# Kernel tuning notes

Hardware: AMD Instinct MI355X
Metric: run time of the kernel (lower is better)

Reference implementation:

```python
import jax, jax.numpy as jnp
import numpy as np

NEG_SLOPE = 0.2
EPS = 1e-16


def sp_gat_layer(h, src, trg, w, a_src, a_trg):
    # h: [N, f_in], w: [H, f_in, f_out], a_src/a_trg: [H, f_out]
    n = h.shape[0]
    h_prime = jnp.einsum('nf,hfo->nho', h, w)            # [N, H, O]
    attn_src = jnp.einsum('nho,ho->nh', h_prime, a_src)  # [N, H]
    attn_trg = jnp.einsum('nho,ho->nh', h_prime, a_trg)  # [N, H]
    e = jax.nn.leaky_relu(attn_src[src] + attn_trg[trg], NEG_SLOPE)  # [E, H]
    e = e - e.max()  # global max-shift, as in the torch code
    exp_e = jnp.exp(e)
    denom = jax.ops.segment_sum(exp_e, trg, num_segments=n)          # [N, H]
    neigh_attn = exp_e / (denom[trg] + EPS)                          # [E, H]
    h_weighted = h_prime[src] * neigh_attn[..., None]                # [E, H, O]
    return jax.ops.segment_sum(h_weighted, trg, num_segments=n)     # [N, H, O]


def run_stack(h, src, trg, params):
    # params: list of (w, a_src, a_trg); last layer mean over heads, others elu+flatten
    n = h.shape[0]
    n_layers = len(params)
    for i, (w, a_src, a_trg) in enumerate(params):
        out = sp_gat_layer(h, src, trg, w, a_src, a_trg)  # [N, H, O]
        if i + 1 == n_layers:
            h = out.mean(axis=1)                          # [N, O]
        else:
            h = jax.nn.elu(out.reshape(n, -1))            # [N, H*O]
    return h


def setup_inputs() -> dict:
    key = jax.random.key(0)
    ks = jax.random.split(key, 24)
    N, E = 60000, 800000
    H, F0, O = 8, 128, 32
    inp = {
        'h0': jax.random.normal(ks[0], (N, F0), jnp.float32),
        'h1': jax.random.normal(ks[1], (N, F0), jnp.float32),
        'src0': jax.random.randint(ks[2], (E,), 0, N),
        'trg0': jax.random.randint(ks[3], (E,), 0, N),
        'src1': jax.random.randint(ks[4], (E,), 0, N),
        'trg1': jax.random.randint(ks[5], (E,), 0, N),
        'w00': jax.random.normal(ks[6], (H, F0, O), jnp.float32) * 0.1,
        'asrc00': jax.random.normal(ks[7], (H, O), jnp.float32) * 0.1,
        'atrg00': jax.random.normal(ks[8], (H, O), jnp.float32) * 0.1,
        'w01': jax.random.normal(ks[9], (H, H * O, O), jnp.float32) * 0.1,
        'asrc01': jax.random.normal(ks[10], (H, O), jnp.float32) * 0.1,
        'atrg01': jax.random.normal(ks[11], (H, O), jnp.float32) * 0.1,
        'w10': jax.random.normal(ks[12], (H, F0, O), jnp.float32) * 0.1,
        'asrc10': jax.random.normal(ks[13], (H, O), jnp.float32) * 0.1,
        'atrg10': jax.random.normal(ks[14], (H, O), jnp.float32) * 0.1,
        'w11': jax.random.normal(ks[15], (H, H * O, O), jnp.float32) * 0.1,
        'asrc11': jax.random.normal(ks[16], (H, O), jnp.float32) * 0.1,
        'atrg11': jax.random.normal(ks[17], (H, O), jnp.float32) * 0.1,
        'fc_w': jax.random.normal(ks[18], (2 * O, 2), jnp.float32) * 0.1,
        'fc_b': jnp.zeros((2,), jnp.float32),
    }
    return inp


N_USER = 50000


def reference(h0, h1, src0, trg0, src1, trg1,
              w00, asrc00, atrg00, w01, asrc01, atrg01,
              w10, asrc10, atrg10, w11, asrc11, atrg11,
              fc_w, fc_b):
    emb0 = run_stack(h0, src0, trg0, [(w00, asrc00, atrg00), (w01, asrc01, atrg01)])
    emb1 = run_stack(h1, src1, trg1, [(w10, asrc10, atrg10), (w11, asrc11, atrg11)])
    ret = jnp.concatenate([emb0[:N_USER], emb1[:N_USER]], axis=-1)  # [n_user, 64]
    logits = ret @ fc_w + fc_b
    return jax.nn.log_softmax(logits, axis=-1)
```

## Files before the change

### kernel.cpp

```cpp
#include <hip/hip_runtime.h>
#include <math.h>

#define H 8
#define O 32
#define C 256
#define CAP 48
#define NEG_SLOPE 0.2f
#define EPS_V 1e-16f
#define LOG2E 1.4426950408889634f

#define W_BKT 128
#define NB_PAD 512
#define BCAP 2048
#define EPB 4096

typedef float f32x4 __attribute__((ext_vector_type(4)));
typedef float f32x2 __attribute__((ext_vector_type(2)));
typedef short bf16x8 __attribute__((ext_vector_type(8)));

__device__ __forceinline__ unsigned short f2bf(float x){
  unsigned u = __float_as_uint(x);
  unsigned r = (u + 0x7fffu + ((u >> 16) & 1u)) >> 16;
  return (unsigned short)r;
}

template<int F>
__device__ __forceinline__ void cvt_a_body(const float* __restrict__ src,
                                           short* __restrict__ dst,
                                           int n_nodes, int t, int total){
  constexpr int KB = F / 8;
  if (t >= total) return;
  int row = t / KB;
  int kb = t - row * KB;
  float v[8];
  if (row < n_nodes){
    const float4 p0 = *(const float4*)(src + (size_t)row * F + kb * 8);
    const float4 p1 = *(const float4*)(src + (size_t)row * F + kb * 8 + 4);
    v[0]=p0.x; v[1]=p0.y; v[2]=p0.z; v[3]=p0.w;
    v[4]=p1.x; v[5]=p1.y; v[6]=p1.z; v[7]=p1.w;
  } else {
    for (int j = 0; j < 8; ++j) v[j] = 0.f;
  }
  bf16x8 o;
  for (int j = 0; j < 8; ++j) o[j] = (short)f2bf(v[j]);
  *(bf16x8*)(dst + (size_t)t * 8) = o;
}

template<int F>
__device__ __forceinline__ void cvt_w_body(const float* __restrict__ w,
                                           short* __restrict__ wb, int t){
  constexpr int KB = F / 8;
  if (t >= 256 * KB) return;
  int c = t & 255, kb = t >> 8;
  int h = c >> 5, o = c & 31;
  bf16x8 out;
  for (int j = 0; j < 8; ++j){
    int f = kb * 8 + j;
    out[j] = (short)f2bf(w[((size_t)h * F + f) * O + o]);
  }
  *(bf16x8*)(wb + ((size_t)kb * 256 + c) * 8) = out;
}

__device__ void pass1_body(const int* __restrict__ trg, const int* __restrict__ src,
                           unsigned* __restrict__ gbuf, unsigned* __restrict__ gcur,
                           int E, int bx, int tid){
  __shared__ int cnt[NB_PAD];
  __shared__ int offl[NB_PAD];
  __shared__ unsigned baseg[NB_PAD];
  __shared__ int cur[NB_PAD];
  __shared__ unsigned payload[EPB];

  const int e0 = bx * EPB;
  const int ne = min(EPB, E - e0);
  for (int i = tid; i < NB_PAD; i += 256) cnt[i] = 0;
  __syncthreads();
  for (int i = tid; i < ne; i += 256){
    int t = trg[e0 + i];
    atomicAdd(&cnt[t >> 7], 1);
  }
  __syncthreads();
  for (int i = tid; i < NB_PAD; i += 256){
    int c = cnt[i];
    baseg[i] = c ? atomicAdd(&gcur[i], (unsigned)c) : 0u;
  }
  if (tid < 64){
    int v[8]; int s = 0;
#pragma unroll
    for (int j = 0; j < 8; ++j){ v[j] = cnt[tid * 8 + j]; s += v[j]; }
    int x = s;
#pragma unroll
    for (int d = 1; d < 64; d <<= 1){
      int o = __shfl_up(x, d, 64);
      if (tid >= d) x += o;
    }
    int base = x - s;
#pragma unroll
    for (int j = 0; j < 8; ++j){ offl[tid * 8 + j] = base; base += v[j]; }
  }
  __syncthreads();
  for (int i = tid; i < NB_PAD; i += 256) cur[i] = offl[i];
  __syncthreads();
  for (int i = tid; i < ne; i += 256){
    int t = trg[e0 + i];
    int s = src[e0 + i];
    int b = t >> 7;
    int p = atomicAdd(&cur[b], 1);
    payload[p] = ((unsigned)b << 23) | ((unsigned)(t & 127) << 16) | (unsigned)s;
  }
  __syncthreads();
  for (int i = tid; i < ne; i += 256){
    unsigned v = payload[i];
    unsigned b = v >> 23;
    unsigned pos = baseg[b] + (unsigned)(i - offl[b]);
    if (pos < BCAP) gbuf[(size_t)b * BCAP + pos] = v;
  }
}

__device__ void pass2_body(const unsigned* __restrict__ gbuf,
                           const unsigned* __restrict__ gcur,
                           unsigned short* __restrict__ csrc, int* __restrict__ degv,
                           int N, int bx, int tid){
  __shared__ unsigned short ell[W_BKT * CAP];
  __shared__ int dcnt[W_BKT];
  const int node0 = bx << 7;
  const int nn = min(W_BKT, N - node0);
  const unsigned pat = ((unsigned)N << 16) | (unsigned)N;
  unsigned* e32 = (unsigned*)ell;
  for (int i = tid; i < W_BKT * CAP / 2; i += 256) e32[i] = pat;
  for (int i = tid; i < W_BKT; i += 256) dcnt[i] = 0;
  __syncthreads();
  const int ne = min((int)gcur[bx], BCAP);
  for (int i = tid; i < ne; i += 256){
    unsigned v = gbuf[(size_t)bx * BCAP + i];
    int lt = (v >> 16) & 127;
    int p = atomicAdd(&dcnt[lt], 1);
    if (p < CAP) ell[lt * CAP + p] = (unsigned short)(v & 0xffffu);
  }
  __syncthreads();
  const uint4* s4 = (const uint4*)ell;
  uint4* d4 = (uint4*)(csrc + (size_t)node0 * CAP);
  const int n16 = nn * (CAP / 8);
  for (int i = tid; i < n16; i += 256) d4[i] = s4[i];
  for (int i = tid; i < nn; i += 256) degv[node0 + i] = dcnt[i];
}

template<int F>
__device__ __forceinline__ void gemm_body(
    const short* __restrict__ hb, const short* __restrict__ wb,
    const float* __restrict__ a_src, const float* __restrict__ a_trg,
    unsigned char* __restrict__ hp, float* __restrict__ as_, float* __restrict__ at_,
    int n_nodes, int bx, int tidx){
  constexpr int KB = F / 8;
  const int w = tidx >> 6, l = tidx & 63;
  const int q = l >> 4, m15 = l & 15;
  const int row0 = bx * 32;
  const int ct0 = w * 4;
  float wsv[4], wtv[4];
#pragma unroll
  for (int ct = 0; ct < 4; ++ct){
    int col = (ct0 + ct) * 16 + m15;
    wsv[ct] = a_src[col];
    wtv[ct] = a_trg[col];
  }
  f32x4 acc[2][4] = {};
#pragma unroll
  for (int kk = 0; kk < F / 32; ++kk){
    const int kb0 = kk * 4 + q;
    bf16x8 a0 = *(const bf16x8*)(hb + ((size_t)(row0 + m15) * KB + kb0) * 8);
    bf16x8 a1 = *(const bf16x8*)(hb + ((size_t)(row0 + 16 + m15) * KB + kb0) * 8);
    const short* wp = wb + ((size_t)kb0 * 256 + ct0 * 16 + m15) * 8;
#pragma unroll
    for (int ct = 0; ct < 4; ++ct){
      bf16x8 b = *(const bf16x8*)(wp + ct * 128);
      acc[0][ct] = __builtin_amdgcn_mfma_f32_16x16x32_bf16(a0, b, acc[0][ct], 0, 0, 0);
      acc[1][ct] = __builtin_amdgcn_mfma_f32_16x16x32_bf16(a1, b, acc[1][ct], 0, 0, 0);
    }
  }
#pragma unroll
  for (int rt2 = 0; rt2 < 2; ++rt2){
    int nb = row0 + rt2 * 16 + q * 4;
    float att[4][4] = {};
#pragma unroll
    for (int ct = 0; ct < 4; ++ct){
      int col = (ct0 + ct) * 16 + m15;
      int hi = ct >> 1;
      int p01 = __builtin_amdgcn_cvt_pk_fp8_f32(acc[rt2][ct][0], acc[rt2][ct][1], 0, false);
      int p23 = __builtin_amdgcn_cvt_pk_fp8_f32(acc[rt2][ct][2], acc[rt2][ct][3], 0, false);
      unsigned char qb[4] = {(unsigned char)(p01 & 0xff),
                             (unsigned char)((p01 >> 8) & 0xff),
                             (unsigned char)(p23 & 0xff),
                             (unsigned char)((p23 >> 8) & 0xff)};
#pragma unroll
      for (int r = 0; r < 4; ++r){
        int n = nb + r;
        if (n < n_nodes) hp[(size_t)n * C + col] = qb[r];
        float vr = acc[rt2][ct][r];
        att[r][hi]     = fmaf(vr, wsv[ct], att[r][hi]);
        att[r][2 + hi] = fmaf(vr, wtv[ct], att[r][2 + hi]);
      }
    }
#pragma unroll
    for (int r = 0; r < 4; ++r)
#pragma unroll
      for (int k = 0; k < 4; ++k){
        float v = att[r][k];
        v += __shfl_xor(v, 1, 64);
        v += __shfl_xor(v, 2, 64);
        v += __shfl_xor(v, 4, 64);
        v += __shfl_xor(v, 8, 64);
        att[r][k] = v;
      }
    if (m15 == 0){
      int h0i = 2 * w;
#pragma unroll
      for (int r = 0; r < 4; ++r){
        int n = nb + r;
        if (n < n_nodes){
          as_[n * H + h0i]     = att[r][0] * LOG2E;
          as_[n * H + h0i + 1] = att[r][1] * LOG2E;
          at_[n * H + h0i]     = att[r][2] * LOG2E;
          at_[n * H + h0i + 1] = att[r][3] * LOG2E;
        }
      }
    }
  }
}

__device__ __forceinline__ float gather_accum(
    const unsigned char* __restrict__ hp,
    const float* __restrict__ as_, float ath,
    const unsigned short* __restrict__ row, int deg, int l, int head,
    f32x2 (&acc)[4]){
  int degR = (deg + 7) & ~7;
  float dsum = 0.f;
  for (int jb = 0; jb < degR; jb += 8){
    ushort4 s4a = *(const ushort4*)(row + jb);
    ushort4 s4b = *(const ushort4*)(row + jb + 4);
    int ss[8] = {s4a.x, s4a.y, s4a.z, s4a.w, s4b.x, s4b.y, s4b.z, s4b.w};
    float xa[8];
#pragma unroll
    for (int i = 0; i < 8; ++i) xa[i] = as_[ss[i] * H + head];
    uint2 vv[8];
#pragma unroll
    for (int i = 0; i < 8; ++i)
      vv[i] = *(const uint2*)(hp + (size_t)ss[i] * C + l * 8);
#pragma unroll
    for (int i = 0; i < 8; ++i){
      float x = xa[i] + ath;
      x = fmaxf(x, NEG_SLOPE * x);
      float e = __builtin_amdgcn_exp2f(x);
      dsum += e;
      f32x2 ee = {e, e};
      f32x2 u0 = __builtin_amdgcn_cvt_pk_f32_fp8(vv[i].x, false);
      f32x2 u1 = __builtin_amdgcn_cvt_pk_f32_fp8(vv[i].x, true);
      f32x2 u2 = __builtin_amdgcn_cvt_pk_f32_fp8(vv[i].y, false);
      f32x2 u3 = __builtin_amdgcn_cvt_pk_f32_fp8(vv[i].y, true);
      acc[0] += u0 * ee;
      acc[1] += u1 * ee;
      acc[2] += u2 * ee;
      acc[3] += u3 * ee;
    }
  }
  return dsum;
}

__global__ void prep_kernel(
    const float* __restrict__ h0, const float* __restrict__ h1,
    const float* __restrict__ w000, const float* __restrict__ w100,
    const float* __restrict__ w001, const float* __restrict__ w101,
    const int* __restrict__ t0, const int* __restrict__ t1,
    const int* __restrict__ s0, const int* __restrict__ s1,
    short* __restrict__ hb, short* __restrict__ wb0, short* __restrict__ wb1,
    unsigned* __restrict__ gbuf, unsigned* __restrict__ gcur,
    float* __restrict__ as_,
    int N, int E, int tot_a, int cvtaB, int p1B,
    size_t hbStride, size_t wbStride, size_t asStride){
  int y = blockIdx.y;
  int bx = blockIdx.x;
  int tid = threadIdx.x;
  if (bx < cvtaB){
    cvt_a_body<128>(y ? h1 : h0, hb + (size_t)y * hbStride, N, bx * 256 + tid, tot_a);
    return;
  }
  bx -= cvtaB;
  if (bx < 16){
    cvt_w_body<128>(y ? w100 : w000, wb0 + (size_t)y * wbStride, bx * 256 + tid);
    return;
  }
  bx -= 16;
  if (bx < 32){
    cvt_w_body<256>(y ? w101 : w001, wb1 + (size_t)y * wbStride, bx * 256 + tid);
    return;
  }
  bx -= 32;
  if (bx < p1B){
    pass1_body(y ? t1 : t0, y ? s1 : s0,
               gbuf + (size_t)y * NB_PAD * BCAP, gcur + (size_t)y * NB_PAD,
               E, bx, tid);
    return;
  }
  if (tid < H) as_[y * asStride + (size_t)N * H + tid] = -1e30f;
}

__global__ __launch_bounds__(256) void binfill_gemm0_kernel(
    const unsigned* __restrict__ gbuf, const unsigned* __restrict__ gcur,
    unsigned short* __restrict__ csrc, int* __restrict__ cursor, int N, int NBk,
    const short* __restrict__ hb, const short* __restrict__ wb0,
    const float* __restrict__ aps0, const float* __restrict__ apt0,
    const float* __restrict__ aps1, const float* __restrict__ apt1,
    unsigned char* __restrict__ hp, float* __restrict__ as_, float* __restrict__ at_,
    size_t hbStride, size_t wbStride, size_t hpStride, size_t asStride){
  int y = blockIdx.y;
  int bx = blockIdx.x;
  if (bx < NBk){
    pass2_body(gbuf + (size_t)y * NB_PAD * BCAP, gcur + (size_t)y * NB_PAD,
               csrc + (size_t)y * N * CAP, cursor + (size_t)y * N, N, bx, threadIdx.x);
    return;
  }
  gemm_body<128>(hb + (size_t)y * hbStride, wb0 + (size_t)y * wbStride,
                 y ? aps1 : aps0, y ? apt1 : apt0,
                 hp + (size_t)y * hpStride, as_ + (size_t)y * asStride,
                 at_ + (size_t)y * asStride, N, bx - NBk, threadIdx.x);
}

__global__ __launch_bounds__(256, 8) void gather0_kernel(
    const unsigned char* __restrict__ hp,
    const float* __restrict__ as_, const float* __restrict__ at_,
    const unsigned short* __restrict__ csrc, const int* __restrict__ degv,
    short* __restrict__ outb, int n_nodes, int N,
    size_t hpStride, size_t asStride, size_t hbStride){
  int y = blockIdx.y;
  hp += (size_t)y * hpStride;
  as_ += (size_t)y * asStride;
  at_ += (size_t)y * asStride;
  csrc += (size_t)y * N * CAP;
  degv += (size_t)y * N;
  outb += (size_t)y * hbStride;
  int wpair = (blockIdx.x * 256 + threadIdx.x) >> 6;
  int lane = threadIdx.x & 63;
  int half = lane >> 5;
  int l = lane & 31;
  int node = wpair * 2 + half;
  if (node >= n_nodes) return;
  int head = l >> 2;
  float ath = at_[node * H + head];
  int deg = degv[node];
  deg = (deg > CAP) ? CAP : deg;
  f32x2 acc[4] = {};
  float dsum = gather_accum(hp, as_, ath, csrc + (size_t)node * CAP, deg, l, head, acc);
  float inv = __builtin_amdgcn_rcpf(dsum + EPS_V);
  bf16x8 o;
#pragma unroll
  for (int k = 0; k < 4; ++k){
    float ax = acc[k].x * inv, ay = acc[k].y * inv;
    float rx = (ax > 0.f) ? ax : (__expf(ax) - 1.f);
    float ry = (ay > 0.f) ? ay : (__expf(ay) - 1.f);
    o[2*k]   = (short)f2bf(rx);
    o[2*k+1] = (short)f2bf(ry);
  }
  *(bf16x8*)(outb + ((size_t)node * 32 + l) * 8) = o;
}

__global__ __launch_bounds__(256) void gemm1_kernel(
    const short* __restrict__ hb, const short* __restrict__ wb1,
    const float* __restrict__ aps0, const float* __restrict__ apt0,
    const float* __restrict__ aps1, const float* __restrict__ apt1,
    unsigned char* __restrict__ hp, float* __restrict__ as_, float* __restrict__ at_,
    int N, size_t hbStride, size_t wbStride, size_t hpStride, size_t asStride){
  int y = blockIdx.y;
  gemm_body<256>(hb + (size_t)y * hbStride, wb1 + (size_t)y * wbStride,
                 y ? aps1 : aps0, y ? apt1 : apt0,
                 hp + (size_t)y * hpStride, as_ + (size_t)y * asStride,
                 at_ + (size_t)y * asStride, N, blockIdx.x, threadIdx.x);
}

__global__ __launch_bounds__(256, 8) void gather_fc_kernel(
    const unsigned char* __restrict__ hp, size_t hpStride,
    const float* __restrict__ as_, const float* __restrict__ at_, size_t asStride,
    const unsigned short* __restrict__ csrc, const int* __restrict__ degv, int N,
    const float* __restrict__ fw, const float* __restrict__ fb,
    float* __restrict__ out, int n_user){
  int node = (blockIdx.x * 256 + threadIdx.x) >> 6;
  if (node >= n_user) return;
  int lane = threadIdx.x & 63;
  int half = lane >> 5;
  int l = lane & 31;
  int head = l >> 2;
  const unsigned char* hps = hp + (size_t)half * hpStride;
  const float* ass = as_ + (size_t)half * asStride;
  const float* ats = at_ + (size_t)half * asStride;
  const unsigned short* row = csrc + (size_t)half * N * CAP + (size_t)node * CAP;
  int deg = degv[(size_t)half * N + node];
  deg = (deg > CAP) ? CAP : deg;
  float ath = ats[node * H + head];
  f32x2 acc[4] = {};
  float dsum = gather_accum(hps, ass, ath, row, deg, l, head, acc);
  float inv = __builtin_amdgcn_rcpf(dsum + EPS_V);
#pragma unroll
  for (int k = 0; k < 4; ++k){ acc[k].x *= inv; acc[k].y *= inv; }
#pragma unroll
  for (int mask = 4; mask <= 16; mask <<= 1){
#pragma unroll
    for (int k = 0; k < 4; ++k){
      acc[k].x += __shfl_xor(acc[k].x, mask, 64);
      acc[k].y += __shfl_xor(acc[k].y, mask, 64);
    }
  }
  float p0 = 0.f, p1 = 0.f;
  if (l < 4){
    float v[8] = {acc[0].x, acc[0].y, acc[1].x, acc[1].y,
                  acc[2].x, acc[2].y, acc[3].x, acc[3].y};
#pragma unroll
    for (int j = 0; j < 8; ++j){
      float e = v[j] * 0.125f;
      int d = half * 32 + l * 8 + j;
      p0 = fmaf(e, fw[d * 2 + 0], p0);
      p1 = fmaf(e, fw[d * 2 + 1], p1);
    }
  }
#pragma unroll
  for (int mask = 1; mask <= 32; mask <<= 1){
    p0 += __shfl_xor(p0, mask, 64);
    p1 += __shfl_xor(p1, mask, 64);
  }
  if (lane == 0){
    float l0 = p0 + fb[0], l1 = p1 + fb[1];
    float m = fmaxf(l0, l1);
    float lse = m + logf(expf(l0 - m) + expf(l1 - m));
    out[(size_t)node * 2 + 0] = l0 - lse;
    out[(size_t)node * 2 + 1] = l1 - lse;
  }
}

extern "C" void kernel_launch(void* const* d_in, const int* in_sizes, int n_in,
                              void* d_out, int out_size, void* d_ws, size_t ws_size,
                              hipStream_t stream){
  const float* h0 = (const float*)d_in[0];
  const float* h1 = (const float*)d_in[1];
  const int* src0 = (const int*)d_in[2];
  const int* trg0 = (const int*)d_in[3];
  const int* src1 = (const int*)d_in[4];
  const int* trg1 = (const int*)d_in[5];
  const float* W [2][2] = {{(const float*)d_in[6],  (const float*)d_in[9]},
                           {(const float*)d_in[12], (const float*)d_in[15]}};
  const float* AS[2][2] = {{(const float*)d_in[7],  (const float*)d_in[10]},
                           {(const float*)d_in[13], (const float*)d_in[16]}};
  const float* AT[2][2] = {{(const float*)d_in[8],  (const float*)d_in[11]},
                           {(const float*)d_in[14], (const float*)d_in[17]}};
  const float* fc_w = (const float*)d_in[18];
  const float* fc_b = (const float*)d_in[19];
  float* out = (float*)d_out;

  const int N = in_sizes[0] / 128;
  const int E = in_sizes[2];
  const int n_user = out_size / 2;

  const int RTt = ((N + 31) / 32) * 2;

  const size_t HPS = (size_t)(N + 16) * C;
  const size_t HBS = (size_t)RTt * 32 * 16 * 8;
  const size_t WBS = (size_t)32 * 256 * 8;
  const size_t NHP = (size_t)(N + 1) * H;

  float* ws = (float*)d_ws;
  float* attn_s = ws;  ws += 2 * NHP;
  float* attn_t = ws;  ws += 2 * NHP;
  unsigned char* hp = (unsigned char*)ws;  ws += 2 * HPS / 4;
  short* hb  = (short*)ws;  ws += 2 * HBS / 2;
  short* wb0 = (short*)ws;  ws += 2 * WBS / 2;
  short* wb1 = (short*)ws;  ws += 2 * WBS / 2;
  unsigned short* csrc = (unsigned short*)ws;  ws += (size_t)2 * N * CAP / 2;
  int* cursor = (int*)ws;  ws += (size_t)2 * N;
  unsigned* gbuf = (unsigned*)ws;  ws += (size_t)2 * NB_PAD * BCAP;
  unsigned* gcur = (unsigned*)ws;  ws += 2 * NB_PAD;

  const int gemm_grid = (N + 31) / 32;
  const int tot_a = RTt * 16 * 16;
  const int cvtaB = (tot_a + 255) / 256;
  const int NBk = (N + W_BKT - 1) / W_BKT;
  const int p1B = (E + EPB - 1) / EPB;
  const int gBN = (N * 32 + 255) / 256;
  const int gFC = (n_user * 64 + 255) / 256;

  hipMemsetAsync(gcur, 0, (size_t)2 * NB_PAD * sizeof(unsigned), stream);
  prep_kernel<<<dim3(cvtaB + 16 + 32 + p1B + 1, 2), 256, 0, stream>>>(
      h0, h1, W[0][0], W[1][0], W[0][1], W[1][1],
      trg0, trg1, src0, src1,
      hb, wb0, wb1, gbuf, gcur, attn_s,
      N, E, tot_a, cvtaB, p1B, HBS, WBS, NHP);
  binfill_gemm0_kernel<<<dim3(NBk + gemm_grid, 2), 256, 0, stream>>>(
      gbuf, gcur, csrc, cursor, N, NBk,
      hb, wb0, AS[0][0], AT[0][0], AS[1][0], AT[1][0],
      hp, attn_s, attn_t, HBS, WBS, HPS, NHP);
  gather0_kernel<<<dim3(gBN, 2), 256, 0, stream>>>(
      hp, attn_s, attn_t, csrc, cursor, hb, N, N, HPS, NHP, HBS);
  gemm1_kernel<<<dim3(gemm_grid, 2), 256, 0, stream>>>(
      hb, wb1, AS[0][1], AT[0][1], AS[1][1], AT[1][1],
      hp, attn_s, attn_t, N, HBS, WBS, HPS, NHP);
  gather_fc_kernel<<<gFC, 256, 0, stream>>>(
      hp, HPS, attn_s, attn_t, NHP, csrc, cursor, N, fc_w, fc_b, out, n_user);
}
```

Before: 400.6 us.

## Fuse layer-0 gather aggregation with layer-1 GEMM through shared-memory tile

Merges the layer-0 neighbor aggregation kernel and the layer-1 MFMA GEMM into one kernel. Each block aggregates 32 nodes, writes the ELU'd bf16 features into a swizzled LDS tile, and then runs the 256-wide GEMM straight from LDS. This removes the global round trip of the intermediate activations and one kernel launch. Because the GEMM now reads hp and attention buffers that other blocks' aggregation still needs, the layer-1 outputs go to separate double buffers (hpB and attn B). The cost is lower occupancy from 16KB of LDS per block and a GEMM phase that is serialized behind the irregular gather.

```diff
diff --git a/kernel.cpp b/kernel.cpp
--- a/kernel.cpp
+++ b/kernel.cpp
@@ -272,7 +272,7 @@
     const int* __restrict__ s0, const int* __restrict__ s1,
     short* __restrict__ hb, short* __restrict__ wb0, short* __restrict__ wb1,
     unsigned* __restrict__ gbuf, unsigned* __restrict__ gcur,
-    float* __restrict__ as_,
+    float* __restrict__ asA, float* __restrict__ asB,
     int N, int E, int tot_a, int cvtaB, int p1B,
     size_t hbStride, size_t wbStride, size_t asStride){
   int y = blockIdx.y;
@@ -299,7 +299,10 @@
                E, bx, tid);
     return;
   }
-  if (tid < H) as_[y * asStride + (size_t)N * H + tid] = -1e30f;
+  if (tid < H){
+    asA[y * asStride + (size_t)N * H + tid] = -1e30f;
+    asB[y * asStride + (size_t)N * H + tid] = -1e30f;
+  }
 }
 
 __global__ __launch_bounds__(256) void binfill_gemm0_kernel(
@@ -308,7 +311,7 @@
     const short* __restrict__ hb, const short* __restrict__ wb0,
     const float* __restrict__ aps0, const float* __restrict__ apt0,
     const float* __restrict__ aps1, const float* __restrict__ apt1,
-    unsigned char* __restrict__ hp, float* __restrict__ as_, float* __restrict__ at_,
+    unsigned char* __restrict__ hpA, float* __restrict__ asA, float* __restrict__ atA,
     size_t hbStride, size_t wbStride, size_t hpStride, size_t asStride){
   int y = blockIdx.y;
   int bx = blockIdx.x;
@@ -319,64 +322,140 @@
   }
   gemm_body<128>(hb + (size_t)y * hbStride, wb0 + (size_t)y * wbStride,
                  y ? aps1 : aps0, y ? apt1 : apt0,
-                 hp + (size_t)y * hpStride, as_ + (size_t)y * asStride,
-                 at_ + (size_t)y * asStride, N, bx - NBk, threadIdx.x);
-}
-
-__global__ __launch_bounds__(256, 8) void gather0_kernel(
-    const unsigned char* __restrict__ hp,
-    const float* __restrict__ as_, const float* __restrict__ at_,
+                 hpA + (size_t)y * hpStride, asA + (size_t)y * asStride,
+                 atA + (size_t)y * asStride, N, bx - NBk, threadIdx.x);
+}
+
+__global__ __launch_bounds__(256, 8) void aggmm_kernel(
+    const unsigned char* __restrict__ hpA,
+    const float* __restrict__ asA, const float* __restrict__ atA,
     const unsigned short* __restrict__ csrc, const int* __restrict__ degv,
-    short* __restrict__ outb, int n_nodes, int N,
-    size_t hpStride, size_t asStride, size_t hbStride){
-  int y = blockIdx.y;
-  hp += (size_t)y * hpStride;
-  as_ += (size_t)y * asStride;
-  at_ += (size_t)y * asStride;
-  csrc += (size_t)y * N * CAP;
-  degv += (size_t)y * N;
-  outb += (size_t)y * hbStride;
-  int wpair = (blockIdx.x * 256 + threadIdx.x) >> 6;
-  int lane = threadIdx.x & 63;
-  int half = lane >> 5;
-  int l = lane & 31;
-  int node = wpair * 2 + half;
-  if (node >= n_nodes) return;
-  int head = l >> 2;
-  float ath = at_[node * H + head];
-  int deg = degv[node];
-  deg = (deg > CAP) ? CAP : deg;
-  f32x2 acc[4] = {};
-  float dsum = gather_accum(hp, as_, ath, csrc + (size_t)node * CAP, deg, l, head, acc);
-  float inv = __builtin_amdgcn_rcpf(dsum + EPS_V);
-  bf16x8 o;
-#pragma unroll
-  for (int k = 0; k < 4; ++k){
-    float ax = acc[k].x * inv, ay = acc[k].y * inv;
-    float rx = (ax > 0.f) ? ax : (__expf(ax) - 1.f);
-    float ry = (ay > 0.f) ? ay : (__expf(ay) - 1.f);
-    o[2*k]   = (short)f2bf(rx);
-    o[2*k+1] = (short)f2bf(ry);
-  }
-  *(bf16x8*)(outb + ((size_t)node * 32 + l) * 8) = o;
-}
-
-__global__ __launch_bounds__(256) void gemm1_kernel(
-    const short* __restrict__ hb, const short* __restrict__ wb1,
+    const short* __restrict__ wb1,
     const float* __restrict__ aps0, const float* __restrict__ apt0,
     const float* __restrict__ aps1, const float* __restrict__ apt1,
-    unsigned char* __restrict__ hp, float* __restrict__ as_, float* __restrict__ at_,
-    int N, size_t hbStride, size_t wbStride, size_t hpStride, size_t asStride){
-  int y = blockIdx.y;
-  gemm_body<256>(hb + (size_t)y * hbStride, wb1 + (size_t)y * wbStride,
-                 y ? aps1 : aps0, y ? apt1 : apt0,
-                 hp + (size_t)y * hpStride, as_ + (size_t)y * asStride,
-                 at_ + (size_t)y * asStride, N, blockIdx.x, threadIdx.x);
+    unsigned char* __restrict__ hpB, float* __restrict__ asB, float* __restrict__ atB,
+    int N, size_t hpStride, size_t asStride, size_t wbStride){
+  __shared__ short atile[32 * 256];
+  const int y = blockIdx.y;
+  const unsigned char* hp = hpA + (size_t)y * hpStride;
+  const float* as0_ = asA + (size_t)y * asStride;
+  const float* at0_ = atA + (size_t)y * asStride;
+  const unsigned short* cs = csrc + (size_t)y * (size_t)N * CAP;
+  const int* dg = degv + (size_t)y * N;
+
+  const int tid = threadIdx.x;
+  const int wv = tid >> 6, lane = tid & 63, half = lane >> 5, l = lane & 31;
+  const int head = l >> 2;
+  const int node0 = blockIdx.x * 32;
+
+#pragma unroll
+  for (int p = 0; p < 4; ++p){
+    int nl = wv * 2 + half + p * 8;
+    int node = node0 + nl;
+    if (node < N){
+      float ath = at0_[node * H + head];
+      int deg = dg[node];
+      deg = (deg > CAP) ? CAP : deg;
+      f32x2 acc[4] = {};
+      float dsum = gather_accum(hp, as0_, ath, cs + (size_t)node * CAP, deg, l, head, acc);
+      float inv = __builtin_amdgcn_rcpf(dsum + EPS_V);
+      bf16x8 o;
+#pragma unroll
+      for (int k = 0; k < 4; ++k){
+        float ax = acc[k].x * inv, ay = acc[k].y * inv;
+        float rx = (ax > 0.f) ? ax : (__expf(ax) - 1.f);
+        float ry = (ay > 0.f) ? ay : (__expf(ay) - 1.f);
+        o[2*k]   = (short)f2bf(rx);
+        o[2*k+1] = (short)f2bf(ry);
+      }
+      *(bf16x8*)((char*)atile + nl * 512 + ((l * 16) ^ ((nl & 7) << 4))) = o;
+    }
+  }
+  __syncthreads();
+
+  const int q = lane >> 4, m15 = lane & 15;
+  const int ct0 = wv * 4;
+  const float* a_src = y ? aps1 : aps0;
+  const float* a_trg = y ? apt1 : apt0;
+  float wsv[4], wtv[4];
+#pragma unroll
+  for (int ct = 0; ct < 4; ++ct){
+    int col = (ct0 + ct) * 16 + m15;
+    wsv[ct] = a_src[col];
+    wtv[ct] = a_trg[col];
+  }
+  const short* wb = wb1 + (size_t)y * wbStride;
+  f32x4 acc[2][4] = {};
+  const int key = (m15 & 7) << 4;
+#pragma unroll
+  for (int kk = 0; kk < 8; ++kk){
+    const int kb0 = kk * 4 + q;
+    bf16x8 a0 = *(const bf16x8*)((char*)atile + m15 * 512 + ((kb0 * 16) ^ key));
+    bf16x8 a1 = *(const bf16x8*)((char*)atile + (16 + m15) * 512 + ((kb0 * 16) ^ key));
+    const short* wp = wb + ((size_t)kb0 * 256 + ct0 * 16 + m15) * 8;
+#pragma unroll
+    for (int ct = 0; ct < 4; ++ct){
+      bf16x8 b = *(const bf16x8*)(wp + ct * 128);
+      acc[0][ct] = __builtin_amdgcn_mfma_f32_16x16x32_bf16(a0, b, acc[0][ct], 0, 0, 0);
+      acc[1][ct] = __builtin_amdgcn_mfma_f32_16x16x32_bf16(a1, b, acc[1][ct], 0, 0, 0);
+    }
+  }
+  unsigned char* hpo = hpB + (size_t)y * hpStride;
+  float* aso = asB + (size_t)y * asStride;
+  float* ato = atB + (size_t)y * asStride;
+#pragma unroll
+  for (int rt2 = 0; rt2 < 2; ++rt2){
+    int nb = node0 + rt2 * 16 + q * 4;
+    float att[4][4] = {};
+#pragma unroll
+    for (int ct = 0; ct < 4; ++ct){
+      int col = (ct0 + ct) * 16 + m15;
+      int hi = ct >> 1;
+      int p01 = __builtin_amdgcn_cvt_pk_fp8_f32(acc[rt2][ct][0], acc[rt2][ct][1], 0, false);
+      int p23 = __builtin_amdgcn_cvt_pk_fp8_f32(acc[rt2][ct][2], acc[rt2][ct][3], 0, false);
+      unsigned char qb[4] = {(unsigned char)(p01 & 0xff),
+                             (unsigned char)((p01 >> 8) & 0xff),
+                             (unsigned char)(p23 & 0xff),
+                             (unsigned char)((p23 >> 8) & 0xff)};
+#pragma unroll
+      for (int r = 0; r < 4; ++r){
+        int n = nb + r;
+        if (n < N) hpo[(size_t)n * C + col] = qb[r];
+        float vr = acc[rt2][ct][r];
+        att[r][hi]     = fmaf(vr, wsv[ct], att[r][hi]);
+        att[r][2 + hi] = fmaf(vr, wtv[ct], att[r][2 + hi]);
+      }
+    }
+#pragma unroll
+    for (int r = 0; r < 4; ++r)
+#pragma unroll
+      for (int k = 0; k < 4; ++k){
+        float v = att[r][k];
+        v += __shfl_xor(v, 1, 64);
+        v += __shfl_xor(v, 2, 64);
+        v += __shfl_xor(v, 4, 64);
+        v += __shfl_xor(v, 8, 64);
+        att[r][k] = v;
+      }
+    if (m15 == 0){
+      int h0i = 2 * wv;
+#pragma unroll
+      for (int r = 0; r < 4; ++r){
+        int n = nb + r;
+        if (n < N){
+          aso[n * H + h0i]     = att[r][0] * LOG2E;
+          aso[n * H + h0i + 1] = att[r][1] * LOG2E;
+          ato[n * H + h0i]     = att[r][2] * LOG2E;
+          ato[n * H + h0i + 1] = att[r][3] * LOG2E;
+        }
+      }
+    }
+  }
 }
 
 __global__ __launch_bounds__(256, 8) void gather_fc_kernel(
-    const unsigned char* __restrict__ hp, size_t hpStride,
-    const float* __restrict__ as_, const float* __restrict__ at_, size_t asStride,
+    const unsigned char* __restrict__ hpB, size_t hpStride,
+    const float* __restrict__ asB, const float* __restrict__ atB, size_t asStride,
     const unsigned short* __restrict__ csrc, const int* __restrict__ degv, int N,
     const float* __restrict__ fw, const float* __restrict__ fb,
     float* __restrict__ out, int n_user){
@@ -386,9 +465,9 @@
   int half = lane >> 5;
   int l = lane & 31;
   int head = l >> 2;
-  const unsigned char* hps = hp + (size_t)half * hpStride;
-  const float* ass = as_ + (size_t)half * asStride;
-  const float* ats = at_ + (size_t)half * asStride;
+  const unsigned char* hps = hpB + (size_t)half * hpStride;
+  const float* ass = asB + (size_t)half * asStride;
+  const float* ats = atB + (size_t)half * asStride;
   const unsigned short* row = csrc + (size_t)half * N * CAP + (size_t)node * CAP;
   int deg = degv[(size_t)half * N + node];
   deg = (deg > CAP) ? CAP : deg;
@@ -458,14 +537,17 @@
   const int RTt = ((N + 31) / 32) * 2;
 
   const size_t HPS = (size_t)(N + 16) * C;
-  const size_t HBS = (size_t)RTt * 32 * 16 * 8;
+  const size_t HBS = (size_t)RTt * 16 * 16 * 8;
   const size_t WBS = (size_t)32 * 256 * 8;
   const size_t NHP = (size_t)(N + 1) * H;
 
   float* ws = (float*)d_ws;
-  float* attn_s = ws;  ws += 2 * NHP;
-  float* attn_t = ws;  ws += 2 * NHP;
-  unsigned char* hp = (unsigned char*)ws;  ws += 2 * HPS / 4;
+  float* attn_sA = ws;  ws += 2 * NHP;
+  float* attn_tA = ws;  ws += 2 * NHP;
+  float* attn_sB = ws;  ws += 2 * NHP;
+  float* attn_tB = ws;  ws += 2 * NHP;
+  unsigned char* hpA = (unsigned char*)ws;  ws += 2 * HPS / 4;
+  unsigned char* hpB = (unsigned char*)ws;  ws += 2 * HPS / 4;
   short* hb  = (short*)ws;  ws += 2 * HBS / 2;
   short* wb0 = (short*)ws;  ws += 2 * WBS / 2;
   short* wb1 = (short*)ws;  ws += 2 * WBS / 2;
@@ -479,24 +561,22 @@
   const int cvtaB = (tot_a + 255) / 256;
   const int NBk = (N + W_BKT - 1) / W_BKT;
   const int p1B = (E + EPB - 1) / EPB;
-  const int gBN = (N * 32 + 255) / 256;
   const int gFC = (n_user * 64 + 255) / 256;
 
   hipMemsetAsync(gcur, 0, (size_t)2 * NB_PAD * sizeof(unsigned), stream);
   prep_kernel<<<dim3(cvtaB + 16 + 32 + p1B + 1, 2), 256, 0, stream>>>(
       h0, h1, W[0][0], W[1][0], W[0][1], W[1][1],
       trg0, trg1, src0, src1,
-      hb, wb0, wb1, gbuf, gcur, attn_s,
+      hb, wb0, wb1, gbuf, gcur, attn_sA, attn_sB,
       N, E, tot_a, cvtaB, p1B, HBS, WBS, NHP);
   binfill_gemm0_kernel<<<dim3(NBk + gemm_grid, 2), 256, 0, stream>>>(
       gbuf, gcur, csrc, cursor, N, NBk,
       hb, wb0, AS[0][0], AT[0][0], AS[1][0], AT[1][0],
-      hp, attn_s, attn_t, HBS, WBS, HPS, NHP);
-  gather0_kernel<<<dim3(gBN, 2), 256, 0, stream>>>(
-      hp, attn_s, attn_t, csrc, cursor, hb, N, N, HPS, NHP, HBS);
-  gemm1_kernel<<<dim3(gemm_grid, 2), 256, 0, stream>>>(
-      hb, wb1, AS[0][1], AT[0][1], AS[1][1], AT[1][1],
-      hp, attn_s, attn_t, N, HBS, WBS, HPS, NHP);
+      hpA, attn_sA, attn_tA, HBS, WBS, HPS, NHP);
+  aggmm_kernel<<<dim3(gemm_grid, 2), 256, 0, stream>>>(
+      hpA, attn_sA, attn_tA, csrc, cursor, wb1,
+      AS[0][1], AT[0][1], AS[1][1], AT[1][1],
+      hpB, attn_sB, attn_tB, N, HPS, NHP, WBS);
   gather_fc_kernel<<<gFC, 256, 0, stream>>>(
-      hp, HPS, attn_s, attn_t, NHP, csrc, cursor, N, fc_w, fc_b, out, n_user);
-}
+      hpB, HPS, attn_sB, attn_tB, NHP, csrc, cursor, N, fc_w, fc_b, out, n_user);
+}
```

Result: faster. 377.5 us (-5.8%).
